# Optimization experiments

Hardware: AMD Instinct MI355X
Metric: run time of the kernel (lower is better)

## Reference

```python
import jax, jax.numpy as jnp
import numpy as np

T_FRAMES = 8
N_HEADS = 8
N_GROUPS = 32
EPS = 1e-5


def _group_norm(x, w, b):
    # x: (N, C, L); GroupNorm with 32 groups over (C//32, L)
    N, C, L = x.shape
    xg = x.reshape(N, N_GROUPS, -1)
    m = xg.mean(-1, keepdims=True)
    v = xg.var(-1, keepdims=True)
    xg = (xg - m) / jnp.sqrt(v + EPS)
    return xg.reshape(N, C, L) * w[None, :, None] + b[None, :, None]


def _layer_norm(x, w, b):
    m = x.mean(-1, keepdims=True)
    v = x.var(-1, keepdims=True)
    return (x - m) / jnp.sqrt(v + EPS) * w + b


def _cross_attn(v, l, qw, qb, kw, kb, vw, vb, ow, ob):
    # v: (B, Tq, v_dim), l: (B, Tk, l_dim); weights torch-style (out, in)
    B, Tq, _ = v.shape
    E = qw.shape[0]
    hd = E // N_HEADS
    def split(t):
        return t.reshape(B, -1, N_HEADS, hd).transpose(0, 2, 1, 3)
    q = split((v @ qw.T + qb) * (hd ** -0.5))
    k = split(l @ kw.T + kb)
    val = split(l @ vw.T + vb)
    aw = jnp.einsum('bhqd,bhkd->bhqk', q, k)
    aw = jnp.clip(aw - jnp.max(aw), -50000.0, 50000.0)  # stable_softmax_2d + clamps
    p = jax.nn.softmax(aw, axis=-1)
    o = jnp.einsum('bhqk,bhkd->bhqd', p, val)
    return o.transpose(0, 2, 1, 3).reshape(B, Tq, E) @ ow.T + ob


def _block(v, l, lnvw, lnvb, lnlw, lnlb, qw, qb, kw, kb, vw, vb, ow, ob, gamma):
    # CrossAttentionBlock: residual is on the NORMALIZED v (as in the torch code)
    vn = _layer_norm(v, lnvw, lnvb)
    ln_ = _layer_norm(l, lnlw, lnlb)
    return vn + gamma * _cross_attn(vn, ln_, qw, qb, kw, kb, vw, vb, ow, ob)


def _forward(x, context, gn1_w, gn1_b, gn2_w, gn2_b,
             sa_lnv_w, sa_lnv_b, sa_lnl_w, sa_lnl_b,
             sa_qw, sa_qb, sa_kw, sa_kb, sa_vw, sa_vb, sa_ow, sa_ob, sa_gamma,
             ca_lnv_w, ca_lnv_b, ca_lnl_w, ca_lnl_b,
             ca_qw, ca_qb, ca_kw, ca_kb, ca_vw, ca_vb, ca_ow, ca_ob, ca_gamma):
    BT, C, H, W = x.shape
    T = T_FRAMES
    B = BT // T
    HW = H * W
    # '(b f) c x y -> b c f x y' then 'b c f x y -> (b f) c (x y)' is identity up to flattening spatial
    xn = _group_norm(x.reshape(BT, C, HW), gn1_w, gn1_b)
    xs = xn.reshape(B, T, C, HW).transpose(0, 1, 3, 2)  # (b, f, hw, c)
    outs = []
    for idx in range(T):
        # window_mask row idx has ones at frames [max(0, idx-1), idx]
        frames = np.array([0]) if idx == 0 else np.array([idx - 1, idx])
        xa = xs[:, frames]                                   # (b, nf, hw, c)
        # rearrange 'b f l d -> b (l f) d' : token-major interleave of gathered frames
        xa = xa.transpose(0, 2, 1, 3).reshape(B, HW * frames.shape[0], C)
        outs.append(_block(xs[:, idx], xa,
                           sa_lnv_w, sa_lnv_b, sa_lnl_w, sa_lnl_b,
                           sa_qw, sa_qb, sa_kw, sa_kb, sa_vw, sa_vb, sa_ow, sa_ob, sa_gamma))
    xs = jnp.stack(outs, axis=1) + xs
    xn2 = xs.transpose(0, 1, 3, 2).reshape(BT, C, HW)
    v = _group_norm(xn2, gn2_w, gn2_b).transpose(0, 2, 1)    # ((b f), hw, c)
    ctx = jnp.tile(context, (T, 1, 1))                        # torch .repeat(f,1,1)
    v = _block(v, ctx,
               ca_lnv_w, ca_lnv_b, ca_lnl_w, ca_lnl_b,
               ca_qw, ca_qb, ca_kw, ca_kb, ca_vw, ca_vb, ca_ow, ca_ob, ca_gamma)
    return v.transpose(0, 2, 1).reshape(BT, C, H, W)


def setup_inputs() -> dict:
    key = jax.random.key(0)
    C, LANG, T, B, H, W, NTXT = 512, 512, 8, 2, 32, 32, 77
    ks = jax.random.split(key, 16)
    def lin(k, o, i):
        return jax.random.normal(k, (o, i), jnp.float32) * 0.02
    inp = {
        'x': jax.random.normal(ks[0], (B * T, C, H, W), jnp.float32),
        'context': jax.random.normal(ks[1], (B, NTXT, LANG), jnp.float32),
        'gn1_w': jnp.ones((C,), jnp.float32), 'gn1_b': jnp.zeros((C,), jnp.float32),
        'gn2_w': jnp.ones((C,), jnp.float32), 'gn2_b': jnp.zeros((C,), jnp.float32),
        'sa_lnv_w': jnp.ones((C,), jnp.float32), 'sa_lnv_b': jnp.zeros((C,), jnp.float32),
        'sa_lnl_w': jnp.ones((C,), jnp.float32), 'sa_lnl_b': jnp.zeros((C,), jnp.float32),
        'sa_qw': lin(ks[2], C, C), 'sa_qb': jnp.zeros((C,), jnp.float32),
        'sa_kw': lin(ks[3], C, C), 'sa_kb': jnp.zeros((C,), jnp.float32),
        'sa_vw': lin(ks[4], C, C), 'sa_vb': jnp.zeros((C,), jnp.float32),
        'sa_ow': lin(ks[5], C, C), 'sa_ob': jnp.zeros((C,), jnp.float32),
        'sa_gamma': jnp.full((C,), 1e-4, jnp.float32),
        'ca_lnv_w': jnp.ones((C,), jnp.float32), 'ca_lnv_b': jnp.zeros((C,), jnp.float32),
        'ca_lnl_w': jnp.ones((LANG,), jnp.float32), 'ca_lnl_b': jnp.zeros((LANG,), jnp.float32),
        'ca_qw': lin(ks[6], C, C), 'ca_qb': jnp.zeros((C,), jnp.float32),
        'ca_kw': lin(ks[7], C, LANG), 'ca_kb': jnp.zeros((C,), jnp.float32),
        'ca_vw': lin(ks[8], C, LANG), 'ca_vb': jnp.zeros((C,), jnp.float32),
        'ca_ow': lin(ks[9], C, C), 'ca_ob': jnp.zeros((C,), jnp.float32),
        'ca_gamma': jnp.full((C,), 1e-4, jnp.float32),
    }
    return inp


def reference(x, context, gn1_w, gn1_b, gn2_w, gn2_b,
              sa_lnv_w, sa_lnv_b, sa_lnl_w, sa_lnl_b,
              sa_qw, sa_qb, sa_kw, sa_kb, sa_vw, sa_vb, sa_ow, sa_ob, sa_gamma,
              ca_lnv_w, ca_lnv_b, ca_lnl_w, ca_lnl_b,
              ca_qw, ca_qb, ca_kw, ca_kb, ca_vw, ca_vb, ca_ow, ca_ob, ca_gamma):
    return _forward(x, context, gn1_w, gn1_b, gn2_w, gn2_b,
                    sa_lnv_w, sa_lnv_b, sa_lnl_w, sa_lnl_b,
                    sa_qw, sa_qb, sa_kw, sa_kb, sa_vw, sa_vb, sa_ow, sa_ob, sa_gamma,
                    ca_lnv_w, ca_lnv_b, ca_lnl_w, ca_lnl_b,
                    ca_qw, ca_qb, ca_kw, ca_kb, ca_vw, ca_vb, ca_ow, ca_ob, ca_gamma)
```

## Files before the change

### kernel.cpp

```cpp
#include <hip/hip_runtime.h>

typedef __attribute__((ext_vector_type(8))) short short8;
typedef __attribute__((ext_vector_type(4))) short short4v;
typedef __attribute__((ext_vector_type(4))) float floatx4;

#define MFMA_BF16 __builtin_amdgcn_mfma_f32_16x16x32_bf16
#define LOG2E 1.44269504088896340736f

__device__ inline floatx4 MFMA16(short4v a, short4v b, floatx4 c){
#if defined(__HIP_DEVICE_COMPILE__)
  return __builtin_amdgcn_mfma_f32_16x16x16bf16_1k(a, b, c, 0, 0, 0);
#else
  return c;
#endif
}

__device__ inline void gll16(const unsigned short* g, unsigned short* l){
#if defined(__HIP_DEVICE_COMPILE__)
  __builtin_amdgcn_global_load_lds(
      (const __attribute__((address_space(1))) unsigned int*)g,
      (__attribute__((address_space(3))) unsigned int*)l, 16, 0, 0);
#else
  (void)g; (void)l;
#endif
}

__device__ inline unsigned short f2bf(float x){
  unsigned int u = __float_as_uint(x);
  u += 0x7fffu + ((u >> 16) & 1u);
  return (unsigned short)(u >> 16);
}
__device__ inline unsigned pack_bf(float lo, float hi){
  return __builtin_amdgcn_perm(__float_as_uint(hi), __float_as_uint(lo), 0x07060302u);
}

__device__ inline float wave_sum(float v){
  #pragma unroll
  for(int m=32;m>=1;m>>=1) v += __shfl_xor(v,m);
  return v;
}

__global__ __launch_bounds__(256) void gn1_kernel(const float* __restrict__ x,
    const float* __restrict__ w, const float* __restrict__ b, float* __restrict__ xs){
  int g = blockIdx.x, bt = blockIdx.y, tid = threadIdx.x;
  const float* xp = x + ((size_t)bt*512 + g*16)*1024;
  float s=0.f, s2=0.f;
  #pragma unroll
  for(int it=0; it<16; ++it){
    float4 v = *(const float4*)(xp + it*1024 + tid*4);
    s  += v.x+v.y+v.z+v.w;
    s2 += v.x*v.x+v.y*v.y+v.z*v.z+v.w*v.w;
  }
  __shared__ float red[8];
  s = wave_sum(s); s2 = wave_sum(s2);
  int wid = tid>>6;
  if((tid&63)==0){ red[wid*2]=s; red[wid*2+1]=s2; }
  __syncthreads();
  s  = red[0]+red[2]+red[4]+red[6];
  s2 = red[1]+red[3]+red[5]+red[7];
  float mean = s * (1.f/16384.f);
  float var  = s2 * (1.f/16384.f) - mean*mean;
  float rinv = rsqrtf(var + 1e-5f);
  int c = tid & 15, h0 = tid >> 4;
  float sc = w[g*16+c]*rinv;
  float sh = b[g*16+c] - mean*sc;
  const float* xcol = xp + (size_t)c*1024;
  float* op = xs + (size_t)bt*1024*512 + g*16 + c;
  #pragma unroll 4
  for(int it=0; it<64; ++it){
    int hw = h0 + it*16;
    op[(size_t)hw*512] = xcol[hw]*sc + sh;
  }
}

__global__ __launch_bounds__(256) void ln_dual_kernel(const float* __restrict__ xs,
    const float* __restrict__ lvw, const float* __restrict__ lvb,
    const float* __restrict__ llw, const float* __restrict__ llb,
    float* __restrict__ vn, unsigned short* __restrict__ vnb, unsigned short* __restrict__ lnlb){
  int wid = threadIdx.x>>6, l = threadIdx.x&63;
  size_t row = (size_t)blockIdx.x*4 + wid;
  const float* xp = xs + row*512;
  float4 a = *(const float4*)(xp + l*4);
  float4 c = *(const float4*)(xp + 256 + l*4);
  float s  = a.x+a.y+a.z+a.w + c.x+c.y+c.z+c.w;
  float s2 = a.x*a.x+a.y*a.y+a.z*a.z+a.w*a.w + c.x*c.x+c.y*c.y+c.z*c.z+c.w*c.w;
  s = wave_sum(s); s2 = wave_sum(s2);
  float mean = s*(1.f/512.f);
  float rinv = rsqrtf(s2*(1.f/512.f) - mean*mean + 1e-5f);
  int c0 = l*4, c1 = 256 + l*4;
  float y[8] = {(a.x-mean)*rinv,(a.y-mean)*rinv,(a.z-mean)*rinv,(a.w-mean)*rinv,
                (c.x-mean)*rinv,(c.y-mean)*rinv,(c.z-mean)*rinv,(c.w-mean)*rinv};
  float4 o0, o1;
  o0.x=y[0]*lvw[c0+0]+lvb[c0+0]; o0.y=y[1]*lvw[c0+1]+lvb[c0+1];
  o0.z=y[2]*lvw[c0+2]+lvb[c0+2]; o0.w=y[3]*lvw[c0+3]+lvb[c0+3];
  o1.x=y[4]*lvw[c1+0]+lvb[c1+0]; o1.y=y[5]*lvw[c1+1]+lvb[c1+1];
  o1.z=y[6]*lvw[c1+2]+lvb[c1+2]; o1.w=y[7]*lvw[c1+3]+lvb[c1+3];
  *(float4*)(vn + row*512 + c0) = o0;
  *(float4*)(vn + row*512 + c1) = o1;
  ushort4 h;
  h.x=f2bf(o0.x); h.y=f2bf(o0.y); h.z=f2bf(o0.z); h.w=f2bf(o0.w);
  *(ushort4*)(vnb + row*512 + c0) = h;
  h.x=f2bf(o1.x); h.y=f2bf(o1.y); h.z=f2bf(o1.z); h.w=f2bf(o1.w);
  *(ushort4*)(vnb + row*512 + c1) = h;
  h.x=f2bf(y[0]*llw[c0+0]+llb[c0+0]); h.y=f2bf(y[1]*llw[c0+1]+llb[c0+1]);
  h.z=f2bf(y[2]*llw[c0+2]+llb[c0+2]); h.w=f2bf(y[3]*llw[c0+3]+llb[c0+3]);
  *(ushort4*)(lnlb + row*512 + c0) = h;
  h.x=f2bf(y[4]*llw[c1+0]+llb[c1+0]); h.y=f2bf(y[5]*llw[c1+1]+llb[c1+1]);
  h.z=f2bf(y[6]*llw[c1+2]+llb[c1+2]); h.w=f2bf(y[7]*llw[c1+3]+llb[c1+3]);
  *(ushort4*)(lnlb + row*512 + c1) = h;
}

__global__ __launch_bounds__(256) void gn2_stats_kernel(const float* __restrict__ xs2, float* __restrict__ st){
  int g = blockIdx.x, bt = blockIdx.y, tid = threadIdx.x;
  const float* xp = xs2 + (size_t)bt*1024*512;
  int c4 = (tid&3)*4, h0 = tid>>2;
  float s=0.f, s2=0.f;
  #pragma unroll
  for(int it=0; it<16; ++it){
    int hw = h0 + it*64;
    float4 v = *(const float4*)(xp + (size_t)hw*512 + g*16 + c4);
    s  += v.x+v.y+v.z+v.w;
    s2 += v.x*v.x+v.y*v.y+v.z*v.z+v.w*v.w;
  }
  __shared__ float red[8];
  s = wave_sum(s); s2 = wave_sum(s2);
  int wid = tid>>6;
  if((tid&63)==0){ red[wid*2]=s; red[wid*2+1]=s2; }
  __syncthreads();
  if(tid==0){
    s  = red[0]+red[2]+red[4]+red[6];
    s2 = red[1]+red[3]+red[5]+red[7];
    float mean = s * (1.f/16384.f);
    float var  = s2 * (1.f/16384.f) - mean*mean;
    st[(bt*32+g)*2]   = mean;
    st[(bt*32+g)*2+1] = rsqrtf(var + 1e-5f);
  }
}

__global__ __launch_bounds__(256) void gn2ln_kernel(const float* __restrict__ xs2, const float* __restrict__ st,
    const float* __restrict__ gw, const float* __restrict__ gb,
    const float* __restrict__ lw, const float* __restrict__ lb,
    float* __restrict__ vn2, unsigned short* __restrict__ vn2b){
  int wid = threadIdx.x>>6, l = threadIdx.x&63;
  size_t row = (size_t)blockIdx.x*4 + wid;
  int bt = (int)(row >> 10);
  const float* xp = xs2 + row*512;
  float4 a = *(const float4*)(xp + l*4);
  float4 c = *(const float4*)(xp + 256 + l*4);
  int c0 = l*4, c1 = 256 + l*4;
  int g0 = c0>>4, g1 = c1>>4;
  float m0 = st[(bt*32+g0)*2], r0 = st[(bt*32+g0)*2+1];
  float m1 = st[(bt*32+g1)*2], r1 = st[(bt*32+g1)*2+1];
  float y[8];
  y[0]=(a.x-m0)*r0*gw[c0+0]+gb[c0+0]; y[1]=(a.y-m0)*r0*gw[c0+1]+gb[c0+1];
  y[2]=(a.z-m0)*r0*gw[c0+2]+gb[c0+2]; y[3]=(a.w-m0)*r0*gw[c0+3]+gb[c0+3];
  y[4]=(c.x-m1)*r1*gw[c1+0]+gb[c1+0]; y[5]=(c.y-m1)*r1*gw[c1+1]+gb[c1+1];
  y[6]=(c.z-m1)*r1*gw[c1+2]+gb[c1+2]; y[7]=(c.w-m1)*r1*gw[c1+3]+gb[c1+3];
  float s=0.f, s2=0.f;
  #pragma unroll
  for(int i=0;i<8;++i){ s += y[i]; s2 += y[i]*y[i]; }
  s = wave_sum(s); s2 = wave_sum(s2);
  float mean = s*(1.f/512.f);
  float rinv = rsqrtf(s2*(1.f/512.f) - mean*mean + 1e-5f);
  float4 o0, o1;
  o0.x=(y[0]-mean)*rinv*lw[c0+0]+lb[c0+0]; o0.y=(y[1]-mean)*rinv*lw[c0+1]+lb[c0+1];
  o0.z=(y[2]-mean)*rinv*lw[c0+2]+lb[c0+2]; o0.w=(y[3]-mean)*rinv*lw[c0+3]+lb[c0+3];
  o1.x=(y[4]-mean)*rinv*lw[c1+0]+lb[c1+0]; o1.y=(y[5]-mean)*rinv*lw[c1+1]+lb[c1+1];
  o1.z=(y[6]-mean)*rinv*lw[c1+2]+lb[c1+2]; o1.w=(y[7]-mean)*rinv*lw[c1+3]+lb[c1+3];
  *(float4*)(vn2 + row*512 + c0) = o0;
  *(float4*)(vn2 + row*512 + c1) = o1;
  ushort4 h;
  h.x=f2bf(o0.x); h.y=f2bf(o0.y); h.z=f2bf(o0.z); h.w=f2bf(o0.w);
  *(ushort4*)(vn2b + row*512 + c0) = h;
  h.x=f2bf(o1.x); h.y=f2bf(o1.y); h.z=f2bf(o1.z); h.w=f2bf(o1.w);
  *(ushort4*)(vn2b + row*512 + c1) = h;
}

__global__ __launch_bounds__(256) void ctxln_kernel(const float* __restrict__ ctx,
    const float* __restrict__ lw, const float* __restrict__ lb, unsigned short* __restrict__ out){
  int wid = threadIdx.x>>6, l = threadIdx.x&63;
  int row = blockIdx.x*4 + wid;
  if(row >= 154) return;
  const float* xp = ctx + (size_t)row*512;
  float4 a = *(const float4*)(xp + l*4);
  float4 c = *(const float4*)(xp + 256 + l*4);
  float s  = a.x+a.y+a.z+a.w + c.x+c.y+c.z+c.w;
  float s2 = a.x*a.x+a.y*a.y+a.z*a.z+a.w*a.w + c.x*c.x+c.y*c.y+c.z*c.z+c.w*c.w;
  s = wave_sum(s); s2 = wave_sum(s2);
  float mean = s*(1.f/512.f);
  float rinv = rsqrtf(s2*(1.f/512.f) - mean*mean + 1e-5f);
  int c0 = l*4, c1 = 256 + l*4;
  ushort4 h;
  h.x=f2bf((a.x-mean)*rinv*lw[c0+0]+lb[c0+0]); h.y=f2bf((a.y-mean)*rinv*lw[c0+1]+lb[c0+1]);
  h.z=f2bf((a.z-mean)*rinv*lw[c0+2]+lb[c0+2]); h.w=f2bf((a.w-mean)*rinv*lw[c0+3]+lb[c0+3]);
  *(ushort4*)(out + (size_t)row*512 + c0) = h;
  h.x=f2bf((c.x-mean)*rinv*lw[c1+0]+lb[c1+0]); h.y=f2bf((c.y-mean)*rinv*lw[c1+1]+lb[c1+1]);
  h.z=f2bf((c.z-mean)*rinv*lw[c1+2]+lb[c1+2]); h.w=f2bf((c.w-mean)*rinv*lw[c1+3]+lb[c1+3]);
  *(ushort4*)(out + (size_t)row*512 + c1) = h;
}

__global__ __launch_bounds__(256) void cvtw_kernel(const float* s0, const float* s1, const float* s2,
    const float* s3, const float* s4, const float* s5, const float* s6, const float* s7,
    unsigned short* __restrict__ dst){
  const float* srcs[8] = {s0,s1,s2,s3,s4,s5,s6,s7};
  int w = blockIdx.y;
  const float* src = srcs[w];
  int i = (blockIdx.x*256 + threadIdx.x)*4;
  float4 v = *(const float4*)(src + i);
  ushort4 h; h.x=f2bf(v.x); h.y=f2bf(v.y); h.z=f2bf(v.z); h.w=f2bf(v.w);
  *(ushort4*)(dst + (size_t)w*262144 + i) = h;
}

template<int MODE>
__global__ __launch_bounds__(256) void gemm128_kernel(const unsigned short* __restrict__ A,
    const unsigned short* __restrict__ W, const float* __restrict__ bias, int M, float scale,
    unsigned short* __restrict__ outb, float* __restrict__ outf,
    const float* __restrict__ r1, const float* __restrict__ r2, const float* __restrict__ gamma){
  __shared__ unsigned short Asl[128*64];
  __shared__ unsigned short Wsl[128*64];
  int tid = threadIdx.x, l = tid&63, wid = tid>>6, quad = l>>4, ln16 = l&15;
  int wr = wid>>1, wc = wid&1;
  int m0 = blockIdx.x*128, n0 = blockIdx.y*128;
  const unsigned short* Ag[4];
  const unsigned short* Wg[4];
  unsigned short* Al[4];
  unsigned short* Wl[4];
  #pragma unroll
  for(int i=0;i<4;++i){
    int s = i*256 + tid;
    int row = s>>3, kg = s&7;
    int kgs = kg ^ (row&7);
    int ar = m0+row; if(ar > M-1) ar = M-1;
    Ag[i] = A + (size_t)ar*512 + kgs*8;
    Wg[i] = W + (size_t)(n0+row)*512 + kgs*8;
    Al[i] = Asl + row*64 + kg*8;
    Wl[i] = Wsl + row*64 + kg*8;
  }
  floatx4 acc[4][4];
  #pragma unroll
  for(int mf=0;mf<4;++mf)
    #pragma unroll
    for(int nf=0;nf<4;++nf) acc[mf][nf] = (floatx4){0,0,0,0};
  for(int kt=0; kt<8; ++kt){
    int k0 = kt*64;
    #pragma unroll
    for(int i=0;i<4;++i){
      gll16(Ag[i] + k0, Al[i]);
      gll16(Wg[i] + k0, Wl[i]);
    }
    __syncthreads();
    #pragma unroll
    for(int kk=0; kk<2; ++kk){
      short8 av[4], wv[4];
      #pragma unroll
      for(int mf=0;mf<4;++mf){
        int row = wr*64 + mf*16 + ln16;
        int sread = (kk*4 + quad) ^ (row&7);
        av[mf] = *(const short8*)(Asl + row*64 + sread*8);
      }
      #pragma unroll
      for(int nf=0;nf<4;++nf){
        int row = wc*64 + nf*16 + ln16;
        int sread = (kk*4 + quad) ^ (row&7);
        wv[nf] = *(const short8*)(Wsl + row*64 + sread*8);
      }
      #pragma unroll
      for(int mf=0;mf<4;++mf)
        #pragma unroll
        for(int nf=0;nf<4;++nf)
          acc[mf][nf] = MFMA_BF16(av[mf], wv[nf], acc[mf][nf], 0,0,0);
    }
    __syncthreads();
  }
  #pragma unroll
  for(int mf=0;mf<4;++mf){
    int mb = m0 + wr*64 + mf*16 + quad*4;
    #pragma unroll
    for(int nf=0;nf<4;++nf){
      int col = n0 + wc*64 + nf*16 + ln16;
      float bv = bias[col];
      if(MODE==0){
        #pragma unroll
        for(int r=0;r<4;++r){
          int m = mb + r;
          if(m < M) outb[(size_t)m*512 + col] = f2bf((acc[mf][nf][r] + bv)*scale);
        }
      } else if(MODE==1){
        float gv = gamma[col];
        #pragma unroll
        for(int r=0;r<4;++r){
          size_t ix = (size_t)(mb+r)*512 + col;
          outf[ix] = r1[ix] + r2[ix] + gv*(acc[mf][nf][r] + bv);
        }
      } else if(MODE==2){
        float gv = gamma[col];
        int bt = mb >> 10;
        int hw0 = mb & 1023;
        float4 ov;
        ov.x = r1[(size_t)(mb+0)*512+col] + gv*(acc[mf][nf][0]+bv);
        ov.y = r1[(size_t)(mb+1)*512+col] + gv*(acc[mf][nf][1]+bv);
        ov.z = r1[(size_t)(mb+2)*512+col] + gv*(acc[mf][nf][2]+bv);
        ov.w = r1[(size_t)(mb+3)*512+col] + gv*(acc[mf][nf][3]+bv);
        *(float4*)(outf + (size_t)bt*524288 + (size_t)col*1024 + hw0) = ov;
      } else if(MODE==3){
        int bf = mb >> 10;
        int hw0 = mb & 1023;
        ushort4 h;
        h.x = f2bf(acc[mf][nf][0]+bv); h.y = f2bf(acc[mf][nf][1]+bv);
        h.z = f2bf(acc[mf][nf][2]+bv); h.w = f2bf(acc[mf][nf][3]+bv);
        *(ushort4*)(outb + ((size_t)bf*512 + col)*1024 + hw0) = h;
      } else {
        #pragma unroll
        for(int r=0;r<4;++r){
          int m = mb + r;
          if(m < M){
            int cb = (m >= 77) ? 1 : 0;
            int key = m - 77*cb;
            outb[((size_t)cb*512 + col)*128 + key] = f2bf(acc[mf][nf][r] + bv);
          }
        }
      }
    }
  }
}

__global__ __launch_bounds__(256, 2) void attn_sp_kernel(const unsigned short* __restrict__ Q,
    const unsigned short* __restrict__ K, const unsigned short* __restrict__ VT,
    unsigned short* __restrict__ O){
  int id = blockIdx.x;
  int hb = id & 127, qt = id >> 7;
  int head = hb >> 4, bz = hb & 15;
  int b = bz >> 3, idx = bz & 7;
  int tid = threadIdx.x, wid = tid>>6, l = tid&63, quad = l>>4, ln16 = l&15;
  __shared__ unsigned short vt[2][64*72];
  __shared__ unsigned short kt[2][64*72];
  size_t qbase = (size_t)bz*1024 + qt*256 + wid*64 + ln16;
  short8 qb[4][2];
  #pragma unroll
  for(int grp=0;grp<4;++grp){
    const unsigned short* qp = Q + (qbase + grp*16)*512 + head*64 + quad*8;
    qb[grp][0] = *(const short8*)(qp);
    qb[grp][1] = *(const short8*)(qp + 32);
  }
  floatx4 o[4][4];
  #pragma unroll
  for(int g=0;g<4;++g)
    #pragma unroll
    for(int d=0;d<4;++d) o[g][d] = (floatx4){0,0,0,0};
  float lr[4] = {0.f,0.f,0.f,0.f};
  int nch = idx ? 32 : 16;
  int f0  = idx ? (idx-1) : 0;
  int sr = tid>>2, sc0 = (tid&3)*16;
  short8 pv0, pv1, pk0, pk1;
  {
    const unsigned short* vp = VT + (((size_t)(b*8+f0)*512) + head*64 + sr)*1024 + sc0;
    pv0 = *(const short8*)(vp); pv1 = *(const short8*)(vp + 8);
    const unsigned short* kp = K + (((size_t)(b*8+f0))*1024 + sr)*512 + head*64 + sc0;
    pk0 = *(const short8*)(kp); pk1 = *(const short8*)(kp + 8);
  }
  for(int ch=0; ch<nch; ++ch){
    int bf_ = ch & 1;
    *(short8*)(&vt[bf_][0] + sr*72 + sc0)     = pv0;
    *(short8*)(&vt[bf_][0] + sr*72 + sc0 + 8) = pv1;
    *(short8*)(&kt[bf_][0] + sr*72 + sc0)     = pk0;
    *(short8*)(&kt[bf_][0] + sr*72 + sc0 + 8) = pk1;
    if(ch+1 < nch){
      int f = f0 + ((ch+1)>>4);
      int kk0 = ((ch+1)&15)*64;
      const unsigned short* vp = VT + (((size_t)(b*8+f)*512) + head*64 + sr)*1024 + kk0 + sc0;
      pv0 = *(const short8*)(vp); pv1 = *(const short8*)(vp + 8);
      const unsigned short* kp = K + (((size_t)(b*8+f))*1024 + kk0 + sr)*512 + head*64 + sc0;
      pk0 = *(const short8*)(kp); pk1 = *(const short8*)(kp + 8);
    }
    __syncthreads();
    #pragma unroll
    for(int g=0; g<4; ++g){
      const unsigned short* kr = &kt[bf_][0] + (g*16+ln16)*72 + quad*8;
      short8 k0 = *(const short8*)(kr);
      short8 k1 = *(const short8*)(kr + 32);
      short4v va[4];
      #pragma unroll
      for(int dc=0; dc<4; ++dc)
        va[dc] = *(const short4v*)(&vt[bf_][0] + (dc*16+ln16)*72 + g*16 + quad*4);
      #pragma unroll
      for(int grp=0; grp<4; ++grp){
        floatx4 s = {0,0,0,0};
        s = MFMA_BF16(k0, qb[grp][0], s, 0,0,0);
        s = MFMA_BF16(k1, qb[grp][1], s, 0,0,0);
        float p0 = __builtin_amdgcn_exp2f(s[0]);
        float p1 = __builtin_amdgcn_exp2f(s[1]);
        float p2 = __builtin_amdgcn_exp2f(s[2]);
        float p3 = __builtin_amdgcn_exp2f(s[3]);
        lr[grp] += (p0+p1)+(p2+p3);
        uint2 pu; pu.x = pack_bf(p0,p1); pu.y = pack_bf(p2,p3);
        short4v pb = __builtin_bit_cast(short4v, pu);
        #pragma unroll
        for(int dc=0; dc<4; ++dc)
          o[grp][dc] = MFMA16(va[dc], pb, o[grp][dc]);
      }
    }
  }
  #pragma unroll
  for(int grp=0; grp<4; ++grp){
    float lt = lr[grp];
    lt += __shfl_xor(lt, 16); lt += __shfl_xor(lt, 32);
    float inv = __builtin_amdgcn_rcpf(lt);
    size_t orow = qbase + grp*16;
    unsigned short* op = O + orow*512 + head*64 + quad*4;
    #pragma unroll
    for(int dc=0; dc<4; ++dc){
      uint2 pk;
      pk.x = pack_bf(o[grp][dc][0]*inv, o[grp][dc][1]*inv);
      pk.y = pack_bf(o[grp][dc][2]*inv, o[grp][dc][3]*inv);
      *(uint2*)(op + dc*16) = pk;
    }
  }
}

__global__ __launch_bounds__(256) void attn_ca_kernel(const unsigned short* __restrict__ Q,
    const unsigned short* __restrict__ K2, const unsigned short* __restrict__ V2T,
    unsigned short* __restrict__ O){
  int id = blockIdx.x;
  int hb = id & 127, qt = id >> 7;
  int head = hb >> 4, bt = hb & 15;
  int cb = bt & 1;
  int tid = threadIdx.x, wid = tid>>6, l = tid&63, quad = l>>4, ln16 = l&15;
  __shared__ unsigned short vt[2][64*72];
  __shared__ unsigned short kt[2][64*72];
  size_t qbase = (size_t)bt*1024 + qt*128 + wid*32 + ln16;
  short8 qb[2][2];
  #pragma unroll
  for(int grp=0;grp<2;++grp){
    const unsigned short* qp = Q + (qbase + grp*16)*512 + head*64 + quad*8;
    qb[grp][0] = *(const short8*)(qp);
    qb[grp][1] = *(const short8*)(qp + 32);
  }
  floatx4 o[2][4];
  #pragma unroll
  for(int g=0;g<2;++g)
    #pragma unroll
    for(int d=0;d<4;++d) o[g][d] = (floatx4){0,0,0,0};
  float lr[2] = {0.f,0.f};
  int sr = tid>>2, sc0 = (tid&3)*16;
  short8 pv0, pv1, pk0, pk1;
  {
    const unsigned short* vp = V2T + (((size_t)cb*512) + head*64 + sr)*128 + sc0;
    pv0 = *(const short8*)(vp); pv1 = *(const short8*)(vp + 8);
    const unsigned short* kp = K2 + ((size_t)cb*77 + sr)*512 + head*64 + sc0;
    pk0 = *(const short8*)(kp); pk1 = *(const short8*)(kp + 8);
  }
  for(int ch=0; ch<2; ++ch){
    int bf_ = ch & 1;
    int kk0 = ch*64;
    *(short8*)(&vt[bf_][0] + sr*72 + sc0)     = pv0;
    *(short8*)(&vt[bf_][0] + sr*72 + sc0 + 8) = pv1;
    *(short8*)(&kt[bf_][0] + sr*72 + sc0)     = pk0;
    *(short8*)(&kt[bf_][0] + sr*72 + sc0 + 8) = pk1;
    if(ch == 0){
      const unsigned short* vp = V2T + (((size_t)cb*512) + head*64 + sr)*128 + 64 + sc0;
      pv0 = *(const short8*)(vp); pv1 = *(const short8*)(vp + 8);
      const unsigned short* kp = K2 + ((size_t)cb*77 + 64 + sr)*512 + head*64 + sc0;
      pk0 = *(const short8*)(kp); pk1 = *(const short8*)(kp + 8);
    }
    __syncthreads();
    #pragma unroll
    for(int g=0; g<4; ++g){
      int kg = kk0 + g*16 + quad*4;
      const unsigned short* kr = &kt[bf_][0] + (g*16+ln16)*72 + quad*8;
      short8 k0 = *(const short8*)(kr);
      short8 k1 = *(const short8*)(kr + 32);
      short4v va[4];
      #pragma unroll
      for(int dc=0; dc<4; ++dc)
        va[dc] = *(const short4v*)(&vt[bf_][0] + (dc*16+ln16)*72 + g*16 + quad*4);
      #pragma unroll
      for(int grp=0; grp<2; ++grp){
        floatx4 s = {0,0,0,0};
        s = MFMA_BF16(k0, qb[grp][0], s, 0,0,0);
        s = MFMA_BF16(k1, qb[grp][1], s, 0,0,0);
        float p0 = (kg+0 < 77) ? __builtin_amdgcn_exp2f(s[0]) : 0.f;
        float p1 = (kg+1 < 77) ? __builtin_amdgcn_exp2f(s[1]) : 0.f;
        float p2 = (kg+2 < 77) ? __builtin_amdgcn_exp2f(s[2]) : 0.f;
        float p3 = (kg+3 < 77) ? __builtin_amdgcn_exp2f(s[3]) : 0.f;
        lr[grp] += (p0+p1)+(p2+p3);
        uint2 pu; pu.x = pack_bf(p0,p1); pu.y = pack_bf(p2,p3);
        short4v pb = __builtin_bit_cast(short4v, pu);
        #pragma unroll
        for(int dc=0; dc<4; ++dc)
          o[grp][dc] = MFMA16(va[dc], pb, o[grp][dc]);
      }
    }
  }
  #pragma unroll
  for(int grp=0; grp<2; ++grp){
    float lt = lr[grp];
    lt += __shfl_xor(lt, 16); lt += __shfl_xor(lt, 32);
    float inv = __builtin_amdgcn_rcpf(lt);
    size_t orow = qbase + grp*16;
    unsigned short* op = O + orow*512 + head*64 + quad*4;
    #pragma unroll
    for(int dc=0; dc<4; ++dc){
      uint2 pk;
      pk.x = pack_bf(o[grp][dc][0]*inv, o[grp][dc][1]*inv);
      pk.y = pack_bf(o[grp][dc][2]*inv, o[grp][dc][3]*inv);
      *(uint2*)(op + dc*16) = pk;
    }
  }
}

extern "C" void kernel_launch(void* const* d_in, const int* in_sizes, int n_in,
                              void* d_out, int out_size, void* d_ws, size_t ws_size,
                              hipStream_t stream) {
  const float* x        = (const float*)d_in[0];
  const float* ctx      = (const float*)d_in[1];
  const float* gn1w     = (const float*)d_in[2];
  const float* gn1b     = (const float*)d_in[3];
  const float* gn2w     = (const float*)d_in[4];
  const float* gn2b     = (const float*)d_in[5];
  const float* sa_lnv_w = (const float*)d_in[6];
  const float* sa_lnv_b = (const float*)d_in[7];
  const float* sa_lnl_w = (const float*)d_in[8];
  const float* sa_lnl_b = (const float*)d_in[9];
  const float* sa_qw    = (const float*)d_in[10];
  const float* sa_qb    = (const float*)d_in[11];
  const float* sa_kw    = (const float*)d_in[12];
  const float* sa_kb    = (const float*)d_in[13];
  const float* sa_vw    = (const float*)d_in[14];
  const float* sa_vb    = (const float*)d_in[15];
  const float* sa_ow    = (const float*)d_in[16];
  const float* sa_ob    = (const float*)d_in[17];
  const float* sa_gamma = (const float*)d_in[18];
  const float* ca_lnv_w = (const float*)d_in[19];
  const float* ca_lnv_b = (const float*)d_in[20];
  const float* ca_lnl_w = (const float*)d_in[21];
  const float* ca_lnl_b = (const float*)d_in[22];
  const float* ca_qw    = (const float*)d_in[23];
  const float* ca_qb    = (const float*)d_in[24];
  const float* ca_kw    = (const float*)d_in[25];
  const float* ca_kb    = (const float*)d_in[26];
  const float* ca_vw    = (const float*)d_in[27];
  const float* ca_vb    = (const float*)d_in[28];
  const float* ca_ow    = (const float*)d_in[29];
  const float* ca_ob    = (const float*)d_in[30];
  const float* ca_gamma = (const float*)d_in[31];

  const size_t BIGF = (size_t)16384*512*4;
  const size_t BIGH = (size_t)16384*512*2;
  char* w8 = (char*)d_ws;
  float*          xs   = (float*)(w8);
  float*          vn   = (float*)(w8 + BIGF);
  unsigned short* vnb  = (unsigned short*)(w8 + 2*BIGF);
  unsigned short* lnlb = (unsigned short*)(w8 + 2*BIGF + 1*BIGH);
  unsigned short* Qb   = (unsigned short*)(w8 + 2*BIGF + 2*BIGH);
  unsigned short* Kb   = (unsigned short*)(w8 + 2*BIGF + 3*BIGH);
  unsigned short* VTb  = (unsigned short*)(w8 + 2*BIGF + 4*BIGH);
  unsigned short* Ob   = (unsigned short*)(w8 + 2*BIGF + 5*BIGH);
  char* small = w8 + 2*BIGF + 6*BIGH;
  float*          st   = (float*)(small);
  unsigned short* ctxb = (unsigned short*)(small + 4096);
  unsigned short* Wb   = (unsigned short*)(small + 4096 + 157696);
  unsigned short* K2b  = (unsigned short*)(w8);
  unsigned short* V2T  = (unsigned short*)(w8 + 1048576);
  float* xs2 = (float*)d_out;

  const float QS = 0.125f * LOG2E;

  cvtw_kernel<<<dim3(256,8),256,0,stream>>>(sa_qw, sa_kw, sa_vw, sa_ow, ca_qw, ca_kw, ca_vw, ca_ow, Wb);
  gn1_kernel<<<dim3(32,16),256,0,stream>>>(x, gn1w, gn1b, xs);
  ln_dual_kernel<<<4096,256,0,stream>>>(xs, sa_lnv_w, sa_lnv_b, sa_lnl_w, sa_lnl_b, vn, vnb, lnlb);
  gemm128_kernel<0><<<dim3(128,4),256,0,stream>>>(vnb,  Wb+0*262144, sa_qb, 16384, QS,   Qb, nullptr, nullptr, nullptr, nullptr);
  gemm128_kernel<0><<<dim3(128,4),256,0,stream>>>(lnlb, Wb+1*262144, sa_kb, 16384, 1.0f, Kb, nullptr, nullptr, nullptr, nullptr);
  gemm128_kernel<3><<<dim3(128,4),256,0,stream>>>(lnlb, Wb+2*262144, sa_vb, 16384, 1.0f, VTb, nullptr, nullptr, nullptr, nullptr);
  attn_sp_kernel<<<512,256,0,stream>>>(Qb, Kb, VTb, Ob);
  gemm128_kernel<1><<<dim3(128,4),256,0,stream>>>(Ob, Wb+3*262144, sa_ob, 16384, 1.0f, nullptr, xs2, xs, vn, sa_gamma);
  gn2_stats_kernel<<<dim3(32,16),256,0,stream>>>(xs2, st);
  gn2ln_kernel<<<4096,256,0,stream>>>(xs2, st, gn2w, gn2b, ca_lnv_w, ca_lnv_b, vn, vnb);
  ctxln_kernel<<<39,256,0,stream>>>(ctx, ca_lnl_w, ca_lnl_b, ctxb);
  gemm128_kernel<0><<<dim3(2,4),256,0,stream>>>(ctxb, Wb+5*262144, ca_kb, 154, 1.0f, K2b, nullptr, nullptr, nullptr, nullptr);
  (void)hipMemsetAsync(V2T, 0, (size_t)2*512*128*2, stream);
  gemm128_kernel<4><<<dim3(2,4),256,0,stream>>>(ctxb, Wb+6*262144, ca_vb, 154, 1.0f, V2T, nullptr, nullptr, nullptr, nullptr);
  gemm128_kernel<0><<<dim3(128,4),256,0,stream>>>(vnb, Wb+4*262144, ca_qb, 16384, QS, Qb, nullptr, nullptr, nullptr, nullptr);
  attn_ca_kernel<<<1024,256,0,stream>>>(Qb, K2b, V2T, Ob);
  gemm128_kernel<2><<<dim3(128,4),256,0,stream>>>(Ob, Wb+7*262144, ca_ob, 16384, 1.0f, nullptr, (float*)d_out, vn, nullptr, ca_gamma);
}
```

Before: 457.1 us.

## Double-buffer GEMM LDS tiles and fuse GroupNorm stats into output-projection epilogue

```diff
diff --git a/kernel.cpp b/kernel.cpp
--- a/kernel.cpp
+++ b/kernel.cpp
@@ -110,33 +110,6 @@
   *(ushort4*)(lnlb + row*512 + c1) = h;
 }
 
-__global__ __launch_bounds__(256) void gn2_stats_kernel(const float* __restrict__ xs2, float* __restrict__ st){
-  int g = blockIdx.x, bt = blockIdx.y, tid = threadIdx.x;
-  const float* xp = xs2 + (size_t)bt*1024*512;
-  int c4 = (tid&3)*4, h0 = tid>>2;
-  float s=0.f, s2=0.f;
-  #pragma unroll
-  for(int it=0; it<16; ++it){
-    int hw = h0 + it*64;
-    float4 v = *(const float4*)(xp + (size_t)hw*512 + g*16 + c4);
-    s  += v.x+v.y+v.z+v.w;
-    s2 += v.x*v.x+v.y*v.y+v.z*v.z+v.w*v.w;
-  }
-  __shared__ float red[8];
-  s = wave_sum(s); s2 = wave_sum(s2);
-  int wid = tid>>6;
-  if((tid&63)==0){ red[wid*2]=s; red[wid*2+1]=s2; }
-  __syncthreads();
-  if(tid==0){
-    s  = red[0]+red[2]+red[4]+red[6];
-    s2 = red[1]+red[3]+red[5]+red[7];
-    float mean = s * (1.f/16384.f);
-    float var  = s2 * (1.f/16384.f) - mean*mean;
-    st[(bt*32+g)*2]   = mean;
-    st[(bt*32+g)*2+1] = rsqrtf(var + 1e-5f);
-  }
-}
-
 __global__ __launch_bounds__(256) void gn2ln_kernel(const float* __restrict__ xs2, const float* __restrict__ st,
     const float* __restrict__ gw, const float* __restrict__ gb,
     const float* __restrict__ lw, const float* __restrict__ lb,
@@ -149,8 +122,12 @@
   float4 c = *(const float4*)(xp + 256 + l*4);
   int c0 = l*4, c1 = 256 + l*4;
   int g0 = c0>>4, g1 = c1>>4;
-  float m0 = st[(bt*32+g0)*2], r0 = st[(bt*32+g0)*2+1];
-  float m1 = st[(bt*32+g1)*2], r1 = st[(bt*32+g1)*2+1];
+  float sm0 = st[(bt*32+g0)*2], sq0 = st[(bt*32+g0)*2+1];
+  float sm1 = st[(bt*32+g1)*2], sq1 = st[(bt*32+g1)*2+1];
+  float m0 = sm0*(1.f/16384.f);
+  float r0 = rsqrtf(sq0*(1.f/16384.f) - m0*m0 + 1e-5f);
+  float m1 = sm1*(1.f/16384.f);
+  float r1 = rsqrtf(sq1*(1.f/16384.f) - m1*m1 + 1e-5f);
   float y[8];
   y[0]=(a.x-m0)*r0*gw[c0+0]+gb[c0+0]; y[1]=(a.y-m0)*r0*gw[c0+1]+gb[c0+1];
   y[2]=(a.z-m0)*r0*gw[c0+2]+gb[c0+2]; y[3]=(a.w-m0)*r0*gw[c0+3]+gb[c0+3];
@@ -216,8 +193,8 @@
     const unsigned short* __restrict__ W, const float* __restrict__ bias, int M, float scale,
     unsigned short* __restrict__ outb, float* __restrict__ outf,
     const float* __restrict__ r1, const float* __restrict__ r2, const float* __restrict__ gamma){
-  __shared__ unsigned short Asl[128*64];
-  __shared__ unsigned short Wsl[128*64];
+  __shared__ unsigned short Asl[2][128*64];
+  __shared__ unsigned short Wsl[2][128*64];
   int tid = threadIdx.x, l = tid&63, wid = tid>>6, quad = l>>4, ln16 = l&15;
   int wr = wid>>1, wc = wid&1;
   int m0 = blockIdx.x*128, n0 = blockIdx.y*128;
@@ -233,22 +210,30 @@
     int ar = m0+row; if(ar > M-1) ar = M-1;
     Ag[i] = A + (size_t)ar*512 + kgs*8;
     Wg[i] = W + (size_t)(n0+row)*512 + kgs*8;
-    Al[i] = Asl + row*64 + kg*8;
-    Wl[i] = Wsl + row*64 + kg*8;
+    Al[i] = &Asl[0][0] + row*64 + kg*8;
+    Wl[i] = &Wsl[0][0] + row*64 + kg*8;
   }
   floatx4 acc[4][4];
   #pragma unroll
   for(int mf=0;mf<4;++mf)
     #pragma unroll
     for(int nf=0;nf<4;++nf) acc[mf][nf] = (floatx4){0,0,0,0};
+  #pragma unroll
+  for(int i=0;i<4;++i){ gll16(Ag[i], Al[i]); gll16(Wg[i], Wl[i]); }
   for(int kt=0; kt<8; ++kt){
-    int k0 = kt*64;
-    #pragma unroll
-    for(int i=0;i<4;++i){
-      gll16(Ag[i] + k0, Al[i]);
-      gll16(Wg[i] + k0, Wl[i]);
-    }
-    __syncthreads();
+    int cur = kt&1;
+    if(kt<7){
+      int k0n = (kt+1)*64, off = (cur^1)*8192;
+      #pragma unroll
+      for(int i=0;i<4;++i){ gll16(Ag[i]+k0n, Al[i]+off); gll16(Wg[i]+k0n, Wl[i]+off); }
+      asm volatile("s_waitcnt vmcnt(8)" ::: "memory");
+    } else {
+      asm volatile("s_waitcnt vmcnt(0)" ::: "memory");
+    }
+    __builtin_amdgcn_s_barrier();
+    __builtin_amdgcn_sched_barrier(0);
+    const unsigned short* Ab = &Asl[cur][0];
+    const unsigned short* Wbb = &Wsl[cur][0];
     #pragma unroll
     for(int kk=0; kk<2; ++kk){
       short8 av[4], wv[4];
@@ -256,13 +241,13 @@
       for(int mf=0;mf<4;++mf){
         int row = wr*64 + mf*16 + ln16;
         int sread = (kk*4 + quad) ^ (row&7);
-        av[mf] = *(const short8*)(Asl + row*64 + sread*8);
+        av[mf] = *(const short8*)(Ab + row*64 + sread*8);
       }
       #pragma unroll
       for(int nf=0;nf<4;++nf){
         int row = wc*64 + nf*16 + ln16;
         int sread = (kk*4 + quad) ^ (row&7);
-        wv[nf] = *(const short8*)(Wsl + row*64 + sread*8);
+        wv[nf] = *(const short8*)(Wbb + row*64 + sread*8);
       }
       #pragma unroll
       for(int mf=0;mf<4;++mf)
@@ -270,7 +255,43 @@
         for(int nf=0;nf<4;++nf)
           acc[mf][nf] = MFMA_BF16(av[mf], wv[nf], acc[mf][nf], 0,0,0);
     }
-    __syncthreads();
+    if(kt<7){
+      __builtin_amdgcn_sched_barrier(0);
+      __builtin_amdgcn_s_barrier();
+    }
+  }
+  if(MODE==1){
+    float gs[4]={0,0,0,0}, gs2[4]={0,0,0,0};
+    #pragma unroll
+    for(int mf=0;mf<4;++mf){
+      int mb = m0 + wr*64 + mf*16 + quad*4;
+      #pragma unroll
+      for(int nf=0;nf<4;++nf){
+        int col = n0 + wc*64 + nf*16 + ln16;
+        float bv = bias[col];
+        float gv = gamma[col];
+        #pragma unroll
+        for(int r=0;r<4;++r){
+          size_t ix = (size_t)(mb+r)*512 + col;
+          float val = r1[ix] + r2[ix] + gv*(acc[mf][nf][r] + bv);
+          outf[ix] = val;
+          gs[nf] += val; gs2[nf] += val*val;
+        }
+      }
+    }
+    float* stats = (float*)outb;
+    int btq = m0 >> 10;
+    #pragma unroll
+    for(int nf=0;nf<4;++nf){
+      float sv  = wave_sum(gs[nf]);
+      float sv2 = wave_sum(gs2[nf]);
+      if(l==0){
+        int g = (n0 + wc*64 + nf*16) >> 4;
+        atomicAdd(&stats[(btq*32+g)*2],   sv);
+        atomicAdd(&stats[(btq*32+g)*2+1], sv2);
+      }
+    }
+    return;
   }
   #pragma unroll
   for(int mf=0;mf<4;++mf){
@@ -284,13 +305,6 @@
         for(int r=0;r<4;++r){
           int m = mb + r;
           if(m < M) outb[(size_t)m*512 + col] = f2bf((acc[mf][nf][r] + bv)*scale);
-        }
-      } else if(MODE==1){
-        float gv = gamma[col];
-        #pragma unroll
-        for(int r=0;r<4;++r){
-          size_t ix = (size_t)(mb+r)*512 + col;
-          outf[ix] = r1[ix] + r2[ix] + gv*(acc[mf][nf][r] + bv);
         }
       } else if(MODE==2){
         float gv = gamma[col];
@@ -309,7 +323,7 @@
         h.x = f2bf(acc[mf][nf][0]+bv); h.y = f2bf(acc[mf][nf][1]+bv);
         h.z = f2bf(acc[mf][nf][2]+bv); h.w = f2bf(acc[mf][nf][3]+bv);
         *(ushort4*)(outb + ((size_t)bf*512 + col)*1024 + hw0) = h;
-      } else {
+      } else if(MODE==4){
         #pragma unroll
         for(int r=0;r<4;++r){
           int m = mb + r;
@@ -572,8 +586,8 @@
   gemm128_kernel<0><<<dim3(128,4),256,0,stream>>>(lnlb, Wb+1*262144, sa_kb, 16384, 1.0f, Kb, nullptr, nullptr, nullptr, nullptr);
   gemm128_kernel<3><<<dim3(128,4),256,0,stream>>>(lnlb, Wb+2*262144, sa_vb, 16384, 1.0f, VTb, nullptr, nullptr, nullptr, nullptr);
   attn_sp_kernel<<<512,256,0,stream>>>(Qb, Kb, VTb, Ob);
-  gemm128_kernel<1><<<dim3(128,4),256,0,stream>>>(Ob, Wb+3*262144, sa_ob, 16384, 1.0f, nullptr, xs2, xs, vn, sa_gamma);
-  gn2_stats_kernel<<<dim3(32,16),256,0,stream>>>(xs2, st);
+  (void)hipMemsetAsync(st, 0, 4096, stream);
+  gemm128_kernel<1><<<dim3(128,4),256,0,stream>>>(Ob, Wb+3*262144, sa_ob, 16384, 1.0f, (unsigned short*)st, xs2, xs, vn, sa_gamma);
   gn2ln_kernel<<<4096,256,0,stream>>>(xs2, st, gn2w, gn2b, ca_lnv_w, ca_lnv_b, vn, vnb);
   ctxln_kernel<<<39,256,0,stream>>>(ctx, ca_lnl_w, ca_lnl_b, ctxb);
   gemm128_kernel<0><<<dim3(2,4),256,0,stream>>>(ctxb, Wb+5*262144, ca_kb, 154, 1.0f, K2b, nullptr, nullptr, nullptr, nullptr);
```

Result: faster. 431.8 us (-5.5%).
